# Optimization experiments

Hardware: AMD Instinct MI355X
Metric: run time of the kernel (lower is better)

Reference implementation:

```python
import jax, jax.numpy as jnp
import numpy as np

B, S, D = 4096, 64, 512  # batch, seq_len, input_size == d_model
EPS = 1e-8  # torch F.cosine_similarity default eps


def _cosine_sim(a, b):
    dot = jnp.sum(a * b, axis=-1)
    na = jnp.sqrt(jnp.sum(a * a, axis=-1))
    nb = jnp.sqrt(jnp.sum(b * b, axis=-1))
    return dot / (jnp.maximum(na, EPS) * jnp.maximum(nb, EPS))


def setup_inputs() -> dict:
    key = jax.random.key(0)
    ks = jax.random.split(key, 12)
    w = lambda k, o, i_: (jax.random.normal(k, (o, i_), jnp.float32) / np.sqrt(i_)).astype(jnp.float32)
    return {
        "i": 5,
        "src": jax.random.normal(ks[0], (B, S, D), jnp.float32),
        "enc_memory": jax.random.normal(ks[1], (S, B, 2 * D), jnp.float32),
        "prev_prediction": jax.random.normal(ks[2], (B, D), jnp.float32),
        "source_vector": jax.random.normal(ks[3], (B, D), jnp.float32),
        "Wfg_w": w(ks[4], D, 2 * D + 2), "Wfg_b": jnp.zeros((D,), jnp.float32),
        "Wig_w": w(ks[5], D, 2 * D + 2), "Wig_b": jnp.zeros((D,), jnp.float32),
        "Wogb_w": w(ks[6], D, D), "Wogb_b": jnp.zeros((D,), jnp.float32),
        "WogA_w": w(ks[7], D, D), "WogA_b": jnp.zeros((D,), jnp.float32),
        "Wctb_w": w(ks[8], D, D), "Wctb_b": jnp.zeros((D,), jnp.float32),
        "final_w": w(ks[9], 1, D), "final_b": jnp.zeros((1,), jnp.float32),
    }


def reference(i, src, enc_memory, prev_prediction, source_vector,
              Wfg_w, Wfg_b, Wig_w, Wig_b, Wogb_w, Wogb_b,
              WogA_w, WogA_b, Wctb_w, Wctb_b, final_w, final_b):
    A = prev_prediction                 # [B, D]
    Bv = src[:, i]                      # [B, D]
    Dv = A - Bv                         # [B, D]
    prev_cur = _cosine_sim(A, Bv)       # [B]
    prev_tot = _cosine_sim(A, source_vector)  # [B]
    I = jnp.concatenate([enc_memory[i], prev_cur[:, None], prev_tot[:, None]], axis=1)  # [B, 2D+2]
    fg = jax.nn.sigmoid(I @ Wfg_w.T + Wfg_b)
    ig = jax.nn.sigmoid(I @ Wig_w.T + Wig_b)
    og = jax.nn.sigmoid((Bv @ Wogb_w.T + Wogb_b) + (A @ WogA_w.T + WogA_b))
    ct = fg * A + ig * jnp.tanh(Bv @ Wctb_w.T + Wctb_b)
    ht = og * jax.nn.sigmoid(ct)
    score = jax.nn.sigmoid(ht @ final_w.T + final_b)  # [B, 1]
    out = A - Dv * score                # broadcast [B,1] over [B,D]
    return (out, score)
```

## Files before the change

kernel.cpp:

```cpp
#include <hip/hip_runtime.h>
#include <hip/hip_bf16.h>
#include <stdint.h>

#define NB 4096
#define NS 64
#define ND 512
#define EPSV 1e-8f

typedef float f32x4 __attribute__((ext_vector_type(4)));
typedef short bf16x8 __attribute__((ext_vector_type(8)));

__device__ __forceinline__ short f2bf(float f) {
    union { float f; unsigned u; } v; v.f = f;
    unsigned r = v.u + 0x7fffu + ((v.u >> 16) & 1u);
    return (short)(r >> 16);
}
__device__ __forceinline__ float bf2f(short s) {
    union { unsigned u; float f; } v; v.u = ((unsigned)(unsigned short)s) << 16;
    return v.f;
}
__device__ __forceinline__ float sigm(float x) { return 1.0f / (1.0f + expf(-x)); }

__global__ __launch_bounds__(256) void prep_all(
    const int* __restrict__ ip, const float* __restrict__ src,
    const float* __restrict__ Aa, const float* __restrict__ sv,
    const float* __restrict__ enc,
    const float* __restrict__ Wfg, const float* __restrict__ Wig,
    const float* __restrict__ Wogb, const float* __restrict__ WogA,
    const float* __restrict__ Wctb,
    short* __restrict__ X1, short* __restrict__ X2,
    short* __restrict__ W1, short* __restrict__ Wog, short* __restrict__ Wct,
    float* __restrict__ pcpt, float* __restrict__ wtail)
{
    const int tid  = threadIdx.x;
    const int t    = blockIdx.x * 256 + tid;
    const int wid  = t >> 6;
    const int lane = tid & 63;
    const int i    = *ip;

    {
        const int b = wid;
        const float* Arow = Aa + (size_t)b * ND;
        const float* Brow = src + ((size_t)b * NS + i) * ND;
        const float* Srow = sv + (size_t)b * ND;
        short* x2row = X2 + (size_t)b * 1024;

        float dab = 0.f, daa = 0.f, dbb = 0.f, das = 0.f, dss = 0.f;
        #pragma unroll
        for (int c = 0; c < 2; ++c) {
            const int d0 = c * 256 + lane * 4;
            f32x4 a  = *(const f32x4*)(Arow + d0);
            f32x4 bv = *(const f32x4*)(Brow + d0);
            f32x4 s  = *(const f32x4*)(Srow + d0);
            #pragma unroll
            for (int j = 0; j < 4; ++j) {
                dab += a[j] * bv[j];
                daa += a[j] * a[j];
                dbb += bv[j] * bv[j];
                das += a[j] * s[j];
                dss += s[j] * s[j];
            }
            short4 qb, qa;
            qb.x = f2bf(bv[0]); qb.y = f2bf(bv[1]); qb.z = f2bf(bv[2]); qb.w = f2bf(bv[3]);
            qa.x = f2bf(a[0]);  qa.y = f2bf(a[1]);  qa.z = f2bf(a[2]);  qa.w = f2bf(a[3]);
            *(short4*)(x2row + d0) = qb;
            *(short4*)(x2row + 512 + d0) = qa;
        }
        #pragma unroll
        for (int off = 32; off; off >>= 1) {
            dab += __shfl_xor(dab, off);
            daa += __shfl_xor(daa, off);
            dbb += __shfl_xor(dbb, off);
            das += __shfl_xor(das, off);
            dss += __shfl_xor(dss, off);
        }
        if (lane == 0) {
            const float na = fmaxf(sqrtf(daa), EPSV);
            const float nb = fmaxf(sqrtf(dbb), EPSV);
            const float ns = fmaxf(sqrtf(dss), EPSV);
            pcpt[b * 2]     = dab / (na * nb);
            pcpt[b * 2 + 1] = das / (na * ns);
        }
    }
    {
        const float* encs = enc + (size_t)i * NB * 1024;
        #pragma unroll
        for (int c = 0; c < 4; ++c) {
            const size_t e4 = (size_t)c * 262144 + t;
            f32x4 v = *(const f32x4*)(encs + e4 * 4);
            short4 q;
            q.x = f2bf(v[0]); q.y = f2bf(v[1]); q.z = f2bf(v[2]); q.w = f2bf(v[3]);
            *(short4*)(X1 + e4 * 4) = q;
        }
    }
    #pragma unroll 1
    for (int idx = t; idx < 1837056; idx += 262144) {
        if (idx < 1048576) {
            const int n = idx >> 10, k = idx & 1023;
            const float v = (n < 512) ? Wfg[(size_t)n * 1026 + k] : Wig[(size_t)(n - 512) * 1026 + k];
            W1[idx] = f2bf(v);
        } else if (idx < 1572864) {
            const int j = idx - 1048576;
            const int n = j >> 10, k = j & 1023;
            const float v = (k < 512) ? Wogb[(size_t)n * 512 + k] : WogA[(size_t)n * 512 + (k - 512)];
            Wog[j] = f2bf(v);
        } else if (idx < 1835008) {
            const int j = idx - 1572864;
            Wct[j] = f2bf(Wctb[j]);
        } else {
            const int tt = idx - 1835008;
            const int r = tt >> 9, d = tt & 511;
            const float v = (r < 2) ? Wfg[(size_t)d * 1026 + 1024 + r]
                                    : Wig[(size_t)d * 1026 + 1024 + (r - 2)];
            wtail[tt] = v;
        }
    }
}

__global__ __launch_bounds__(256, 4) void gemm_bt(
    const short* __restrict__ X1v, const short* __restrict__ W1v,
    const short* __restrict__ X2v, const short* __restrict__ Wogv,
    const short* __restrict__ Wctv,
    short* __restrict__ Gfi, short* __restrict__ Gog, short* __restrict__ Gct)
{
    __shared__ __align__(16) short As[64 * 64];
    __shared__ __align__(16) short Bs[128 * 64];

    const int h = blockIdx.x;
    const int x = h & 7, q = h >> 3;
    const short *Xp, *Wp;
    short* Gp;
    int bx, by, wss, gs, nkt;
    if (q < 64)      { bx = x * 8 + (q >> 3);              by = q & 7;        Xp = X1v; Wp = W1v;  Gp = Gfi; wss = 1024; gs = 1024; nkt = 16; }
    else if (q < 96) { const int j = q - 64; bx = x * 8 + (j >> 2); by = j & 3; Xp = X2v; Wp = Wogv; Gp = Gog; wss = 1024; gs = 512;  nkt = 16; }
    else             { const int j = q - 96; bx = x * 8 + (j >> 2); by = j & 3; Xp = X2v; Wp = Wctv; Gp = Gct; wss = 512;  gs = 512;  nkt = 8;  }

    const int tid = threadIdx.x;
    const int w = tid >> 6, lane = tid & 63;
    const int wm = w >> 1, wn = w & 1;
    const int lr = lane & 15, lg = lane >> 4;
    const int swz = (lr & 7) << 4;

    const size_t ldx = 2048;
    const size_t ldw = (size_t)wss * 2;
    const char* Xb = (const char*)Xp + (size_t)bx * 64 * ldx;
    const char* Wb = (const char*)Wp + (size_t)by * 128 * ldw;

    f32x4 acc[2][4];
    #pragma unroll
    for (int mi = 0; mi < 2; ++mi)
        #pragma unroll
        for (int ni = 0; ni < 4; ++ni)
            acc[mi][ni] = f32x4{0.f, 0.f, 0.f, 0.f};

    for (int kt = 0; kt < nkt; ++kt) {
        __syncthreads();
        #pragma unroll
        for (int s = 0; s < 2; ++s) {
            const int seg = (s * 4 + w) * 1024;
            const int linear = seg + lane * 16;
            const int row = linear >> 7;
            const int kbs = (linear & 127) ^ ((row & 7) << 4);
            __builtin_amdgcn_global_load_lds(
                (const __attribute__((address_space(1))) void*)(Xb + (size_t)row * ldx + (size_t)kt * 128 + kbs),
                (__attribute__((address_space(3))) void*)((char*)As + seg),
                16, 0, 0);
        }
        #pragma unroll
        for (int s = 0; s < 4; ++s) {
            const int seg = (s * 4 + w) * 1024;
            const int linear = seg + lane * 16;
            const int row = linear >> 7;
            const int kbs = (linear & 127) ^ ((row & 7) << 4);
            __builtin_amdgcn_global_load_lds(
                (const __attribute__((address_space(1))) void*)(Wb + (size_t)row * ldw + (size_t)kt * 128 + kbs),
                (__attribute__((address_space(3))) void*)((char*)Bs + seg),
                16, 0, 0);
        }
        __syncthreads();
        #pragma unroll
        for (int ks = 0; ks < 2; ++ks) {
            bf16x8 af[2], bfr[4];
            #pragma unroll
            for (int mi = 0; mi < 2; ++mi)
                af[mi] = *(const bf16x8*)((const char*)As + (wm * 32 + mi * 16 + lr) * 128 + ((ks * 64 + lg * 16) ^ swz));
            #pragma unroll
            for (int ni = 0; ni < 4; ++ni)
                bfr[ni] = *(const bf16x8*)((const char*)Bs + (wn * 64 + ni * 16 + lr) * 128 + ((ks * 64 + lg * 16) ^ swz));
            #pragma unroll
            for (int mi = 0; mi < 2; ++mi)
                #pragma unroll
                for (int ni = 0; ni < 4; ++ni)
                    acc[mi][ni] = __builtin_amdgcn_mfma_f32_16x16x32_bf16(af[mi], bfr[ni], acc[mi][ni], 0, 0, 0);
        }
    }

    short* Grow = Gp + ((size_t)bx * 64 + wm * 32) * gs + by * 128 + wn * 64;
    #pragma unroll
    for (int mi = 0; mi < 2; ++mi)
        #pragma unroll
        for (int ni = 0; ni < 4; ++ni)
            #pragma unroll
            for (int r = 0; r < 4; ++r)
                Grow[(size_t)(mi * 16 + lg * 4 + r) * gs + ni * 16 + lr] = f2bf(acc[mi][ni][r]);
}

__global__ __launch_bounds__(256) void finish_k(
    const int* __restrict__ ip, const short* __restrict__ X2,
    const short* __restrict__ Gfi, const short* __restrict__ Gog, const short* __restrict__ Gct,
    const float* __restrict__ pcpt, const float* __restrict__ wtail,
    const float* __restrict__ bfg, const float* __restrict__ big,
    const float* __restrict__ bogb, const float* __restrict__ bogA, const float* __restrict__ bctb,
    const float* __restrict__ fw, const float* __restrict__ fb,
    float* __restrict__ out)
{
    const int w = threadIdx.x >> 6, lane = threadIdx.x & 63;
    const int b = blockIdx.x * 4 + w;
    const int d = lane * 8;
    const float pc = pcpt[b * 2], pt = pcpt[b * 2 + 1];

    bf16x8 vfg = *(const bf16x8*)(Gfi + (size_t)b * 1024 + d);
    bf16x8 vig = *(const bf16x8*)(Gfi + (size_t)b * 1024 + 512 + d);
    bf16x8 vog = *(const bf16x8*)(Gog + (size_t)b * 512 + d);
    bf16x8 vct = *(const bf16x8*)(Gct + (size_t)b * 512 + d);
    bf16x8 vb8 = *(const bf16x8*)(X2 + (size_t)b * 1024 + d);
    bf16x8 va8 = *(const bf16x8*)(X2 + (size_t)b * 1024 + 512 + d);

    float hsum = 0.f;
    float av[8], bvv[8];
    #pragma unroll
    for (int c = 0; c < 2; ++c) {
        const int d0 = d + c * 4;
        f32x4 c1 = *(const f32x4*)(bfg + d0);
        f32x4 c2 = *(const f32x4*)(big + d0);
        f32x4 c3 = *(const f32x4*)(bogb + d0);
        f32x4 c4 = *(const f32x4*)(bogA + d0);
        f32x4 c5 = *(const f32x4*)(bctb + d0);
        f32x4 vfw = *(const f32x4*)(fw + d0);
        f32x4 w0 = *(const f32x4*)(wtail + d0);
        f32x4 w1 = *(const f32x4*)(wtail + 512 + d0);
        f32x4 w2 = *(const f32x4*)(wtail + 1024 + d0);
        f32x4 w3 = *(const f32x4*)(wtail + 1536 + d0);
        #pragma unroll
        for (int j = 0; j < 4; ++j) {
            const int e = c * 4 + j;
            const float a  = bf2f(va8[e]);
            const float bv = bf2f(vb8[e]);
            const float fg = sigm(bf2f(vfg[e]) + c1[j] + pc * w0[j] + pt * w1[j]);
            const float ig = sigm(bf2f(vig[e]) + c2[j] + pc * w2[j] + pt * w3[j]);
            const float og = sigm(bf2f(vog[e]) + c3[j] + c4[j]);
            const float ct = fg * a + ig * tanhf(bf2f(vct[e]) + c5[j]);
            const float ht = og * sigm(ct);
            hsum += ht * vfw[j];
            av[e] = a; bvv[e] = bv;
        }
    }
    #pragma unroll
    for (int off = 32; off; off >>= 1) hsum += __shfl_xor(hsum, off);
    const float score = sigm(hsum + fb[0]);
    #pragma unroll
    for (int c = 0; c < 2; ++c) {
        f32x4 o;
        #pragma unroll
        for (int j = 0; j < 4; ++j) {
            const float a = av[c * 4 + j];
            o[j] = a - (a - bvv[c * 4 + j]) * score;
        }
        *(f32x4*)(out + (size_t)b * ND + d + c * 4) = o;
    }
    if (lane == 0) out[(size_t)NB * ND + b] = score;
}

extern "C" void kernel_launch(void* const* d_in, const int* in_sizes, int n_in,
                              void* d_out, int out_size, void* d_ws, size_t ws_size,
                              hipStream_t stream) {
    const int*   ip    = (const int*)d_in[0];
    const float* src   = (const float*)d_in[1];
    const float* enc   = (const float*)d_in[2];
    const float* prev  = (const float*)d_in[3];
    const float* sv    = (const float*)d_in[4];
    const float* Wfg_w = (const float*)d_in[5];
    const float* Wfg_b = (const float*)d_in[6];
    const float* Wig_w = (const float*)d_in[7];
    const float* Wig_b = (const float*)d_in[8];
    const float* Wogb_w = (const float*)d_in[9];
    const float* Wogb_b = (const float*)d_in[10];
    const float* WogA_w = (const float*)d_in[11];
    const float* WogA_b = (const float*)d_in[12];
    const float* Wctb_w = (const float*)d_in[13];
    const float* Wctb_b = (const float*)d_in[14];
    const float* fw    = (const float*)d_in[15];
    const float* fb    = (const float*)d_in[16];

    char* ws = (char*)d_ws;
    short* X1   = (short*)(ws + 0);
    short* X2   = (short*)(ws + 8388608);
    short* W1   = (short*)(ws + 16777216);
    short* Wog  = (short*)(ws + 18874368);
    short* Wct  = (short*)(ws + 19922944);
    short* Gfi  = (short*)(ws + 20447232);
    short* Gog  = (short*)(ws + 28835840);
    short* Gct  = (short*)(ws + 33030144);
    float* pcpt = (float*)(ws + 37224448);
    float* wtail= (float*)(ws + 37257216);

    prep_all<<<1024, 256, 0, stream>>>(ip, src, prev, sv, enc,
                                       Wfg_w, Wig_w, Wogb_w, WogA_w, Wctb_w,
                                       X1, X2, W1, Wog, Wct, pcpt, wtail);
    gemm_bt<<<1024, 256, 0, stream>>>(X1, W1, X2, Wog, Wct, Gfi, Gog, Gct);
    finish_k<<<1024, 256, 0, stream>>>(ip, X2, Gfi, Gog, Gct, pcpt, wtail,
                                       Wfg_b, Wig_b, Wogb_b, WogA_b, Wctb_b,
                                       fw, fb, (float*)d_out);
}
```

Measured before the change: 50.53 us.

## Double-buffer LDS tiles in GEMM to overlap global loads with MFMA

Doubles the shared-memory A/B tile buffers and prefetches the next K tile via global_load_lds while computing on the current one, with one barrier per iteration instead of two. The goal is to hide global load latency behind MFMA work. LDS per block doubles to 48KB, and the occupancy hint drops from 4 to 3 blocks, which may reduce latency hiding across blocks. Correctness relies on the single trailing barrier also waiting for the async LDS loads to complete.

```diff
diff --git a/kernel.cpp b/kernel.cpp
--- a/kernel.cpp
+++ b/kernel.cpp
@@ -117,14 +117,38 @@
     }
 }
 
-__global__ __launch_bounds__(256, 4) void gemm_bt(
+#define STAGE2(aoff, boff, ktv)                                                                     \
+    do {                                                                                            \
+        _Pragma("unroll")                                                                           \
+        for (int s = 0; s < 2; ++s) {                                                               \
+            const int seg = (s * 4 + w) * 1024;                                                     \
+            const int linear = seg + lane * 16;                                                     \
+            const int row = linear >> 7;                                                            \
+            const int kbs = (linear & 127) ^ ((row & 7) << 4);                                      \
+            __builtin_amdgcn_global_load_lds(                                                       \
+                (const __attribute__((address_space(1))) void*)(Xb + (size_t)row * ldx + (size_t)(ktv) * 128 + kbs), \
+                (__attribute__((address_space(3))) void*)((char*)As + (aoff) + seg), 16, 0, 0);     \
+        }                                                                                           \
+        _Pragma("unroll")                                                                           \
+        for (int s = 0; s < 4; ++s) {                                                               \
+            const int seg = (s * 4 + w) * 1024;                                                     \
+            const int linear = seg + lane * 16;                                                     \
+            const int row = linear >> 7;                                                            \
+            const int kbs = (linear & 127) ^ ((row & 7) << 4);                                      \
+            __builtin_amdgcn_global_load_lds(                                                       \
+                (const __attribute__((address_space(1))) void*)(Wb + (size_t)row * ldw + (size_t)(ktv) * 128 + kbs), \
+                (__attribute__((address_space(3))) void*)((char*)Bs + (boff) + seg), 16, 0, 0);     \
+        }                                                                                           \
+    } while (0)
+
+__global__ __launch_bounds__(256, 3) void gemm_bt(
     const short* __restrict__ X1v, const short* __restrict__ W1v,
     const short* __restrict__ X2v, const short* __restrict__ Wogv,
     const short* __restrict__ Wctv,
     short* __restrict__ Gfi, short* __restrict__ Gog, short* __restrict__ Gct)
 {
-    __shared__ __align__(16) short As[64 * 64];
-    __shared__ __align__(16) short Bs[128 * 64];
+    __shared__ __align__(16) short As[2 * 64 * 64];
+    __shared__ __align__(16) short Bs[2 * 128 * 64];
 
     const int h = blockIdx.x;
     const int x = h & 7, q = h >> 3;
@@ -153,46 +177,29 @@
         for (int ni = 0; ni < 4; ++ni)
             acc[mi][ni] = f32x4{0.f, 0.f, 0.f, 0.f};
 
+    STAGE2(0, 0, 0);
+    __syncthreads();
+
     for (int kt = 0; kt < nkt; ++kt) {
-        __syncthreads();
-        #pragma unroll
-        for (int s = 0; s < 2; ++s) {
-            const int seg = (s * 4 + w) * 1024;
-            const int linear = seg + lane * 16;
-            const int row = linear >> 7;
-            const int kbs = (linear & 127) ^ ((row & 7) << 4);
-            __builtin_amdgcn_global_load_lds(
-                (const __attribute__((address_space(1))) void*)(Xb + (size_t)row * ldx + (size_t)kt * 128 + kbs),
-                (__attribute__((address_space(3))) void*)((char*)As + seg),
-                16, 0, 0);
-        }
-        #pragma unroll
-        for (int s = 0; s < 4; ++s) {
-            const int seg = (s * 4 + w) * 1024;
-            const int linear = seg + lane * 16;
-            const int row = linear >> 7;
-            const int kbs = (linear & 127) ^ ((row & 7) << 4);
-            __builtin_amdgcn_global_load_lds(
-                (const __attribute__((address_space(1))) void*)(Wb + (size_t)row * ldw + (size_t)kt * 128 + kbs),
-                (__attribute__((address_space(3))) void*)((char*)Bs + seg),
-                16, 0, 0);
-        }
-        __syncthreads();
+        const int aoff = (kt & 1) * 8192;
+        const int boff = (kt & 1) * 16384;
+        if (kt + 1 < nkt) STAGE2(aoff ^ 8192, boff ^ 16384, kt + 1);
         #pragma unroll
         for (int ks = 0; ks < 2; ++ks) {
             bf16x8 af[2], bfr[4];
             #pragma unroll
             for (int mi = 0; mi < 2; ++mi)
-                af[mi] = *(const bf16x8*)((const char*)As + (wm * 32 + mi * 16 + lr) * 128 + ((ks * 64 + lg * 16) ^ swz));
+                af[mi] = *(const bf16x8*)((const char*)As + aoff + (wm * 32 + mi * 16 + lr) * 128 + ((ks * 64 + lg * 16) ^ swz));
             #pragma unroll
             for (int ni = 0; ni < 4; ++ni)
-                bfr[ni] = *(const bf16x8*)((const char*)Bs + (wn * 64 + ni * 16 + lr) * 128 + ((ks * 64 + lg * 16) ^ swz));
+                bfr[ni] = *(const bf16x8*)((const char*)Bs + boff + (wn * 64 + ni * 16 + lr) * 128 + ((ks * 64 + lg * 16) ^ swz));
             #pragma unroll
             for (int mi = 0; mi < 2; ++mi)
                 #pragma unroll
                 for (int ni = 0; ni < 4; ++ni)
                     acc[mi][ni] = __builtin_amdgcn_mfma_f32_16x16x32_bf16(af[mi], bfr[ni], acc[mi][ni], 0, 0, 0);
         }
+        __syncthreads();
     }
 
     short* Grow = Gp + ((size_t)bx * 64 + wm * 32) * gs + by * 128 + wn * 64;
```

After: 55.35 us. 9.5% more time.

## Fuse finish epilogue into GEMM kernel via per-row-panel atomic counters

Applied to the files above, without the earlier changes.

Merges the finish kernel into the GEMM kernel. Each block signals completion of its 64-row panel with an atomic counter, then spin-waits until all 16 tiles of the panel it needs are done before running the elementwise gate and score epilogue. This removes one kernel launch and lets epilogue work overlap with GEMM tiles still running elsewhere. In exchange it adds a memset, atomics and spin-waiting, and it relies on co-residency of blocks to avoid deadlock (a bounded spin is the only guard).

```diff
diff --git a/kernel.cpp b/kernel.cpp
--- a/kernel.cpp
+++ b/kernel.cpp
@@ -117,11 +117,18 @@
     }
 }
 
-__global__ __launch_bounds__(256, 4) void gemm_bt(
+__global__ __launch_bounds__(256, 4) void gemm_finish(
     const short* __restrict__ X1v, const short* __restrict__ W1v,
     const short* __restrict__ X2v, const short* __restrict__ Wogv,
     const short* __restrict__ Wctv,
-    short* __restrict__ Gfi, short* __restrict__ Gog, short* __restrict__ Gct)
+    short* __restrict__ Gfi, short* __restrict__ Gog, short* __restrict__ Gct,
+    unsigned* __restrict__ cnt,
+    const float* __restrict__ pcpt, const float* __restrict__ wtail,
+    const float* __restrict__ bfg, const float* __restrict__ big,
+    const float* __restrict__ bogb, const float* __restrict__ bogA,
+    const float* __restrict__ bctb,
+    const float* __restrict__ fw, const float* __restrict__ fb,
+    float* __restrict__ out)
 {
     __shared__ __align__(16) short As[64 * 64];
     __shared__ __align__(16) short Bs[128 * 64];
@@ -203,72 +210,80 @@
             #pragma unroll
             for (int r = 0; r < 4; ++r)
                 Grow[(size_t)(mi * 16 + lg * 4 + r) * gs + ni * 16 + lr] = f2bf(acc[mi][ni][r]);
-}
-
-__global__ __launch_bounds__(256) void finish_k(
-    const int* __restrict__ ip, const short* __restrict__ X2,
-    const short* __restrict__ Gfi, const short* __restrict__ Gog, const short* __restrict__ Gct,
-    const float* __restrict__ pcpt, const float* __restrict__ wtail,
-    const float* __restrict__ bfg, const float* __restrict__ big,
-    const float* __restrict__ bogb, const float* __restrict__ bogA, const float* __restrict__ bctb,
-    const float* __restrict__ fw, const float* __restrict__ fb,
-    float* __restrict__ out)
-{
-    const int w = threadIdx.x >> 6, lane = threadIdx.x & 63;
-    const int b = blockIdx.x * 4 + w;
-    const int d = lane * 8;
-    const float pc = pcpt[b * 2], pt = pcpt[b * 2 + 1];
-
-    bf16x8 vfg = *(const bf16x8*)(Gfi + (size_t)b * 1024 + d);
-    bf16x8 vig = *(const bf16x8*)(Gfi + (size_t)b * 1024 + 512 + d);
-    bf16x8 vog = *(const bf16x8*)(Gog + (size_t)b * 512 + d);
-    bf16x8 vct = *(const bf16x8*)(Gct + (size_t)b * 512 + d);
-    bf16x8 vb8 = *(const bf16x8*)(X2 + (size_t)b * 1024 + d);
-    bf16x8 va8 = *(const bf16x8*)(X2 + (size_t)b * 1024 + 512 + d);
-
-    float hsum = 0.f;
-    float av[8], bvv[8];
-    #pragma unroll
-    for (int c = 0; c < 2; ++c) {
-        const int d0 = d + c * 4;
-        f32x4 c1 = *(const f32x4*)(bfg + d0);
-        f32x4 c2 = *(const f32x4*)(big + d0);
-        f32x4 c3 = *(const f32x4*)(bogb + d0);
-        f32x4 c4 = *(const f32x4*)(bogA + d0);
-        f32x4 c5 = *(const f32x4*)(bctb + d0);
-        f32x4 vfw = *(const f32x4*)(fw + d0);
-        f32x4 w0 = *(const f32x4*)(wtail + d0);
-        f32x4 w1 = *(const f32x4*)(wtail + 512 + d0);
-        f32x4 w2 = *(const f32x4*)(wtail + 1024 + d0);
-        f32x4 w3 = *(const f32x4*)(wtail + 1536 + d0);
-        #pragma unroll
-        for (int j = 0; j < 4; ++j) {
-            const int e = c * 4 + j;
-            const float a  = bf2f(va8[e]);
-            const float bv = bf2f(vb8[e]);
-            const float fg = sigm(bf2f(vfg[e]) + c1[j] + pc * w0[j] + pt * w1[j]);
-            const float ig = sigm(bf2f(vig[e]) + c2[j] + pc * w2[j] + pt * w3[j]);
-            const float og = sigm(bf2f(vog[e]) + c3[j] + c4[j]);
-            const float ct = fg * a + ig * tanhf(bf2f(vct[e]) + c5[j]);
-            const float ht = og * sigm(ct);
-            hsum += ht * vfw[j];
-            av[e] = a; bvv[e] = bv;
-        }
-    }
-    #pragma unroll
-    for (int off = 32; off; off >>= 1) hsum += __shfl_xor(hsum, off);
-    const float score = sigm(hsum + fb[0]);
-    #pragma unroll
-    for (int c = 0; c < 2; ++c) {
-        f32x4 o;
-        #pragma unroll
-        for (int j = 0; j < 4; ++j) {
-            const float a = av[c * 4 + j];
-            o[j] = a - (a - bvv[c * 4 + j]) * score;
-        }
-        *(f32x4*)(out + (size_t)b * ND + d + c * 4) = o;
-    }
-    if (lane == 0) out[(size_t)NB * ND + b] = score;
+
+    __syncthreads();
+    if (tid == 0) {
+        __threadfence();
+        atomicAdd(&cnt[bx], 1u);
+    }
+
+    if (tid == 0) {
+        const int fp = h >> 4;
+        unsigned iters = 0;
+        while (__hip_atomic_load(&cnt[fp], __ATOMIC_RELAXED, __HIP_MEMORY_SCOPE_AGENT) < 16u) {
+            __builtin_amdgcn_s_sleep(1);
+            if (++iters > 400000000u) break;
+        }
+        __threadfence();
+    }
+    __syncthreads();
+
+    {
+        const int b = h * 4 + w;
+        const int d = lane * 8;
+        const float pc = pcpt[b * 2], pt = pcpt[b * 2 + 1];
+
+        bf16x8 vfg = *(const bf16x8*)(Gfi + (size_t)b * 1024 + d);
+        bf16x8 vig = *(const bf16x8*)(Gfi + (size_t)b * 1024 + 512 + d);
+        bf16x8 vog = *(const bf16x8*)(Gog + (size_t)b * 512 + d);
+        bf16x8 vct = *(const bf16x8*)(Gct + (size_t)b * 512 + d);
+        bf16x8 vb8 = *(const bf16x8*)(X2v + (size_t)b * 1024 + d);
+        bf16x8 va8 = *(const bf16x8*)(X2v + (size_t)b * 1024 + 512 + d);
+
+        float hsum = 0.f;
+        float av[8], bvv[8];
+        #pragma unroll
+        for (int c = 0; c < 2; ++c) {
+            const int d0 = d + c * 4;
+            f32x4 c1 = *(const f32x4*)(bfg + d0);
+            f32x4 c2 = *(const f32x4*)(big + d0);
+            f32x4 c3 = *(const f32x4*)(bogb + d0);
+            f32x4 c4 = *(const f32x4*)(bogA + d0);
+            f32x4 c5 = *(const f32x4*)(bctb + d0);
+            f32x4 vfw = *(const f32x4*)(fw + d0);
+            f32x4 w0 = *(const f32x4*)(wtail + d0);
+            f32x4 w1 = *(const f32x4*)(wtail + 512 + d0);
+            f32x4 w2 = *(const f32x4*)(wtail + 1024 + d0);
+            f32x4 w3 = *(const f32x4*)(wtail + 1536 + d0);
+            #pragma unroll
+            for (int j = 0; j < 4; ++j) {
+                const int e = c * 4 + j;
+                const float a  = bf2f(va8[e]);
+                const float bv = bf2f(vb8[e]);
+                const float fg = sigm(bf2f(vfg[e]) + c1[j] + pc * w0[j] + pt * w1[j]);
+                const float ig = sigm(bf2f(vig[e]) + c2[j] + pc * w2[j] + pt * w3[j]);
+                const float og = sigm(bf2f(vog[e]) + c3[j] + c4[j]);
+                const float ct = fg * a + ig * tanhf(bf2f(vct[e]) + c5[j]);
+                const float ht = og * sigm(ct);
+                hsum += ht * vfw[j];
+                av[e] = a; bvv[e] = bv;
+            }
+        }
+        #pragma unroll
+        for (int off = 32; off; off >>= 1) hsum += __shfl_xor(hsum, off);
+        const float score = sigm(hsum + fb[0]);
+        #pragma unroll
+        for (int c = 0; c < 2; ++c) {
+            f32x4 o;
+            #pragma unroll
+            for (int j = 0; j < 4; ++j) {
+                const float a = av[c * 4 + j];
+                o[j] = a - (a - bvv[c * 4 + j]) * score;
+            }
+            *(f32x4*)(out + (size_t)b * ND + d + c * 4) = o;
+        }
+        if (lane == 0) out[(size_t)NB * ND + b] = score;
+    }
 }
 
 extern "C" void kernel_launch(void* const* d_in, const int* in_sizes, int n_in,
@@ -303,12 +318,15 @@
     short* Gct  = (short*)(ws + 33030144);
     float* pcpt = (float*)(ws + 37224448);
     float* wtail= (float*)(ws + 37257216);
+    unsigned* cnt = (unsigned*)(ws + 37265408);
+
+    hipMemsetAsync(ws + 37265408, 0, 256, stream);
 
     prep_all<<<1024, 256, 0, stream>>>(ip, src, prev, sv, enc,
                                        Wfg_w, Wig_w, Wogb_w, WogA_w, Wctb_w,
                                        X1, X2, W1, Wog, Wct, pcpt, wtail);
-    gemm_bt<<<1024, 256, 0, stream>>>(X1, W1, X2, Wog, Wct, Gfi, Gog, Gct);
-    finish_k<<<1024, 256, 0, stream>>>(ip, X2, Gfi, Gog, Gct, pcpt, wtail,
-                                       Wfg_b, Wig_b, Wogb_b, WogA_b, Wctb_b,
-                                       fw, fb, (float*)d_out);
-}
+    gemm_finish<<<1024, 256, 0, stream>>>(X1, W1, X2, Wog, Wct, Gfi, Gog, Gct, cnt,
+                                          pcpt, wtail,
+                                          Wfg_b, Wig_b, Wogb_b, WogA_b, Wctb_b,
+                                          fw, fb, (float*)d_out);
+}
```

Measured after the change: 151.7 us. 200% more time.
